# Optimization experiments

Measured on AMD Instinct MI355X. Metric: run time of the kernel, lower is better.

Reference implementation:

```python
import jax, jax.numpy as jnp
import numpy as np

B, INPUT, HIDDEN, MEM, SEQ, THETA, FFEAT = 8, 256, 256, 64, 2048, 2048.0, 64


def _expm(M):
    # scaling-and-squaring Taylor expm in float64 (replaces scipy cont2discrete internals)
    norm = np.linalg.norm(M, 1)
    s = max(0, int(np.ceil(np.log2(max(norm, 1e-16)))) + 1)
    A = M / (2.0 ** s)
    n = M.shape[0]
    E = np.eye(n)
    T = np.eye(n)
    for k in range(1, 30):
        T = T @ A / k
        E = E + T
    for _ in range(s):
        E = E @ E
    return E


def _lmu_fft_kernel(memory_size, theta, seq_len):
    # continuous-time LMU (A, B), discretized with ZOH (dt=1), as in cont2discrete
    Q = np.arange(memory_size, dtype=np.float64).reshape(-1, 1)
    R = (2 * Q + 1) / theta
    i, j = np.meshgrid(Q.ravel(), Q.ravel(), indexing='ij')
    A = R * np.where(i < j, -1.0, (-1.0) ** (i - j + 1))
    Bc = R * (-1.0) ** Q  # [m, 1]
    # ZOH via block matrix exponential: expm([[A,B],[0,0]]) = [[Ad,Bd],[0,I]]
    blk = np.zeros((memory_size + 1, memory_size + 1))
    blk[:memory_size, :memory_size] = A
    blk[:memory_size, memory_size:] = Bc
    M = _expm(blk)
    Ad = jnp.asarray(M[:memory_size, :memory_size], dtype=jnp.float32)
    Bd = jnp.asarray(M[:memory_size, memory_size:], dtype=jnp.float32)  # [m,1]
    # H[:, t] = Ad^t @ Bd
    def step(Ai, _):
        return Ad @ Ai, (Ai @ Bd)[:, 0]
    _, cols = jax.lax.scan(step, jnp.eye(memory_size, dtype=jnp.float32), None, length=seq_len)
    H = cols.T  # [m, S]
    return jnp.fft.rfft(H, n=2 * seq_len, axis=-1)  # [m, S+1] complex64


def setup_inputs() -> dict:
    key = jax.random.key(0)
    k1, k2, k3, k4, k5 = jax.random.split(key, 5)
    x = jax.random.normal(k1, (B, INPUT, SEQ), dtype=jnp.float32)
    Wu_w = jax.random.normal(k2, (FFEAT + HIDDEN, INPUT), dtype=jnp.float32) * (1.0 / np.sqrt(INPUT))
    Wu_b = jax.random.normal(k3, (FFEAT + HIDDEN,), dtype=jnp.float32) * 0.02
    Wh_w = jax.random.normal(k4, (HIDDEN, MEM * FFEAT), dtype=jnp.float32) * (1.0 / np.sqrt(MEM * FFEAT))
    Wh_b = jax.random.normal(k5, (HIDDEN,), dtype=jnp.float32) * 0.02
    fft_H = _lmu_fft_kernel(MEM, THETA, SEQ)
    return {"x": x, "Wu_w": Wu_w, "Wu_b": Wu_b, "Wh_w": Wh_w, "Wh_b": Wh_b, "fft_H": fft_H}


def reference(x, Wu_w, Wu_b, Wh_w, Wh_b, fft_H):
    batch, _, seq_len = x.shape
    hidden = Wh_w.shape[0]
    mem = fft_H.shape[0]
    # 1x1 conv == per-position GEMM
    out = jnp.einsum('oi,bis->bos', Wu_w, x) + Wu_b[None, :, None]  # [B, F+H, S]
    u = jax.nn.relu(out[:, hidden:])                                  # [B, F, S]
    fft_u = jnp.fft.rfft(u, n=2 * seq_len, axis=-1)                   # [B, F, S+1]
    temp = fft_u[:, :, None, :] * fft_H[None, None, :, :]             # [B, F, M, S+1]
    m = jnp.fft.irfft(temp, n=2 * seq_len, axis=-1)[..., :seq_len]    # [B, F, M, S]
    m = m.reshape(batch, -1, seq_len)                                 # [B, F*M, S]
    return jnp.einsum('oc,bcs->bos', Wh_w, m) + Wh_b[None, :, None] + out[:, :hidden]
```

## Files before the change

kernel.cpp:

```cpp
#include <hip/hip_runtime.h>
#include <hip/hip_bf16.h>
#include <math.h>

#define NB 8
#define NIN 256
#define NHID 256
#define NMEM 64
#define NSEQ 2048
#define NFEAT 64
#define NOUTCH 320
#define NFFT 4096
#define KBINS 2049

#define FFTU_SZ (NB * NFEAT * KBINS * 2)
#define FHD_SZ (NMEM * KBINS * 2)
#define TW_SZ (2048 * 2)
#define HBUF_SZ (NMEM * NSEQ)
#define FIXED_F (FFTU_SZ + FHD_SZ + TW_SZ + HBUF_SZ)
#define ZPERO_F (8 * KBINS * 2 * 2)

#define DMM   0
#define DTT0  4225
#define DTT1  8450
#define DEE0  12675
#define DEE1  16900
#define DPW   21125
#define DWV   (DPW + 6 * 4096)
#define DMK2  (DWV + 4096)

#define FIDX(i) ((i) + ((i) >> 5) + ((i) >> 10))
#define FFT_LDS 4240
#define HF_LDS 2120

__device__ __forceinline__ void fft4096_core(float* XR, float* XI,
                                             const float2* TWS, bool inverse) {
#pragma unroll 1
  for (int s = 1; s <= 12; ++s) {
    int half = 1 << (s - 1);
    int shift = 12 - s;
#pragma unroll
    for (int q = 0; q < 8; ++q) {
      int bf = threadIdx.x + q * 256;
      int j = bf & (half - 1);
      int base = ((bf >> (s - 1)) << s) + j;
      float2 w = TWS[j << shift];
      float wr = w.x, wi = inverse ? -w.y : w.y;
      int i0 = FIDX(base), i1 = FIDX(base + half);
      float ar = XR[i0], ai = XI[i0];
      float br = XR[i1], bi = XI[i1];
      float tr = wr * br - wi * bi, ti = wr * bi + wi * br;
      XR[i0] = ar + tr; XI[i0] = ai + ti;
      XR[i1] = ar - tr; XI[i1] = ai - ti;
    }
    __syncthreads();
  }
}

__device__ __forceinline__ void fft2048_core(float* XR, float* XI,
                                             const float2* TWS, bool inverse) {
#pragma unroll 1
  for (int s = 1; s <= 11; ++s) {
    int half = 1 << (s - 1);
    int shift = 12 - s;
#pragma unroll
    for (int q = 0; q < 4; ++q) {
      int bf = threadIdx.x + q * 256;
      int j = bf & (half - 1);
      int base = ((bf >> (s - 1)) << s) + j;
      float2 w = TWS[j << shift];
      float wr = w.x, wi = inverse ? -w.y : w.y;
      int i0 = FIDX(base), i1 = FIDX(base + half);
      float ar = XR[i0], ai = XI[i0];
      float br = XR[i1], bi = XI[i1];
      float tr = wr * br - wi * bi, ti = wr * bi + wi * br;
      XR[i0] = ar + tr; XI[i0] = ai + ti;
      XR[i1] = ar - tr; XI[i1] = ai - ti;
    }
    __syncthreads();
  }
}

__global__ void k0_tw(float2* __restrict__ tw) {
  int m = blockIdx.x * 256 + threadIdx.x;
  if (m < 2048) {
    double ang = -2.0 * 3.14159265358979323846 * (double)m / 4096.0;
    tw[m] = make_float2((float)cos(ang), (float)sin(ang));
  }
}

__global__ __launch_bounds__(256) void kinit(double* __restrict__ D) {
  int e = blockIdx.x * 256 + threadIdx.x;
  if (e < 4225) {
    int i = e / 65, j = e % 65;
    double val = 0.0;
    if (i < 64) {
      double R = (2.0 * i + 1.0) / 2048.0;
      if (j < 64) val = R * ((i < j) ? -1.0 : (((i - j) & 1) ? 1.0 : -1.0));
      else        val = R * ((i & 1) ? -1.0 : 1.0);
    }
    D[DMM + e] = 0.25 * val;
    double id = (i == j) ? 1.0 : 0.0;
    D[DTT0 + e] = id; D[DEE0 + e] = id;
  }
}
__global__ __launch_bounds__(256) void kmm65(const double* __restrict__ A,
                                             const double* __restrict__ B,
                                             double* __restrict__ C,
                                             double* __restrict__ E, double kd) {
  int e = blockIdx.x * 256 + threadIdx.x;
  if (e >= 4225) return;
  int i = e / 65, j = e % 65;
  const double* ar = A + i * 65;
  double dot = 0.0;
  for (int l = 0; l < 65; ++l) dot += ar[l] * B[l * 65 + j];
  dot /= kd;
  C[e] = dot;
  if (E) E[e] += dot;
}
__global__ __launch_bounds__(256) void kext(const double* __restrict__ E,
                                            double* __restrict__ D) {
  int e = blockIdx.x * 256 + threadIdx.x;
  if (e < 4096) {
    int i = e >> 6, j = e & 63;
    D[DPW + e] = (double)(float)E[i * 65 + j];
    D[DMK2 + e] = (i == j) ? 1.0 : 0.0;
  } else if (e < 4160) {
    int j = e - 4096;
    D[DWV + j] = (double)(float)E[j * 65 + 64];
  }
}
__global__ __launch_bounds__(256) void kmm64(const double* __restrict__ A,
                                             const double* __restrict__ B,
                                             double* __restrict__ C) {
  int e = blockIdx.x * 256 + threadIdx.x;
  int i = e >> 6, j = e & 63;
  double dot = 0.0;
  for (int l = 0; l < 64; ++l) dot += A[i * 64 + l] * B[l * 64 + j];
  C[e] = dot;
}
__global__ __launch_bounds__(256) void kwlev(const double* __restrict__ P,
                                             double* __restrict__ W, int b0) {
  int tot = 64 * b0;
  for (int e = threadIdx.x; e < tot; e += 256) {
    int t = e >> 6, i = e & 63;
    double dot = 0.0;
    for (int l = 0; l < 64; ++l) dot += P[i * 64 + l] * W[t * 64 + l];
    W[(size_t)(b0 + t) * 64 + i] = dot;
  }
}
__global__ __launch_bounds__(256) void kmk(const double* __restrict__ Q,
                                           const double* __restrict__ Src,
                                           double* __restrict__ Out) {
  int t = blockIdx.y;
  int e = blockIdx.x * 256 + threadIdx.x;
  int i = e >> 6, j = e & 63;
  const double* B = Src + (size_t)t * 4096;
  double dot = 0.0;
  for (int l = 0; l < 64; ++l) dot += Q[i * 64 + l] * B[l * 64 + j];
  Out[(size_t)t * 4096 + e] = dot;
}

__global__ __launch_bounds__(256) void kB_cols(const double* __restrict__ D,
                                               float* __restrict__ H) {
  const double* W = D + DWV;
  const double* Mrow = D + DMK2 + (size_t)blockIdx.x * 4096;
  __shared__ double Ms[4096];
  __shared__ double WssT[4096];
  const int tid = threadIdx.x;
  for (int e = tid; e < 4096; e += 256) {
    Ms[e] = Mrow[e];
    int r = e >> 6, j = e & 63;
    WssT[j * 64 + r] = W[e];
  }
  __syncthreads();
  const int c0 = blockIdx.x * 64;
  for (int e = tid; e < 4096; e += 256) {
    int i = e >> 6, r = e & 63;
    double dot = 0.0;
#pragma unroll 16
    for (int j = 0; j < 64; ++j) dot += Ms[i * 64 + j] * WssT[j * 64 + r];
    H[(size_t)i * NSEQ + c0 + r] = (float)dot;
  }
}

__global__ __launch_bounds__(256) void kC_fft(const float* __restrict__ H,
                                              const float2* __restrict__ tw,
                                              float* __restrict__ fHd) {
  __shared__ float XR[FFT_LDS], XI[FFT_LDS];
  __shared__ float2 TWS[2048];
  const int tid = threadIdx.x;
  const int mi = blockIdx.x;
  const float* src = H + (size_t)mi * NSEQ;
  for (int i = tid; i < NFFT; i += 256) { XR[FIDX(i)] = 0.f; XI[FIDX(i)] = 0.f; }
  for (int i = tid; i < 2048; i += 256) TWS[i] = tw[i];
  __syncthreads();
  for (int i = tid; i < NSEQ; i += 256) {
    int r = __brev((unsigned)i) >> 20;
    XR[FIDX(r)] = src[i];
  }
  __syncthreads();
  fft4096_core(XR, XI, TWS, false);
  float2* dst = (float2*)fHd + (size_t)mi * KBINS;
  for (int k = tid; k < KBINS; k += 256)
    dst[k] = make_float2(XR[FIDX(k)], XI[FIDX(k)]);
}

__global__ __launch_bounds__(256) void k1t(
    const float* __restrict__ x, const float* __restrict__ Wuw,
    const float* __restrict__ Wub, const float* __restrict__ Whb,
    float* __restrict__ dout, float* __restrict__ ubuf) {
  __shared__ float xs[32][128];
  __shared__ float wsh[32][68];
  const int tid = threadIdx.x;
  const int b = blockIdx.z;
  const int o0 = blockIdx.y * 64;
  const int s0 = blockIdx.x * 128;
  const int sx = tid & 15, oy = tid >> 4;
  float acc[4][8];
#pragma unroll
  for (int j = 0; j < 4; ++j)
#pragma unroll
    for (int l = 0; l < 8; ++l) acc[j][l] = 0.f;

  for (int i0 = 0; i0 < 256; i0 += 32) {
#pragma unroll
    for (int e4 = tid; e4 < 1024; e4 += 256) {
      int ii = e4 >> 5, ss4 = (e4 & 31) << 2;
      float4 v = *(const float4*)&x[(size_t)(b * NIN + i0 + ii) * NSEQ + s0 + ss4];
      *(float4*)&xs[ii][ss4] = v;
    }
#pragma unroll
    for (int e4 = tid; e4 < 512; e4 += 256) {
      int oj = e4 >> 3, ii4 = (e4 & 7) << 2;
      float4 v = *(const float4*)&Wuw[(o0 + oj) * NIN + i0 + ii4];
      wsh[ii4][oj] = v.x; wsh[ii4 + 1][oj] = v.y;
      wsh[ii4 + 2][oj] = v.z; wsh[ii4 + 3][oj] = v.w;
    }
    __syncthreads();
#pragma unroll 8
    for (int kk = 0; kk < 32; ++kk) {
      float4 a = *(const float4*)&wsh[kk][oy * 4];
      float4 b0 = *(const float4*)&xs[kk][sx * 4];
      float4 b1 = *(const float4*)&xs[kk][64 + sx * 4];
      float av[4] = {a.x, a.y, a.z, a.w};
      float bv[8] = {b0.x, b0.y, b0.z, b0.w, b1.x, b1.y, b1.z, b1.w};
#pragma unroll
      for (int j = 0; j < 4; ++j)
#pragma unroll
        for (int l = 0; l < 8; ++l) acc[j][l] = fmaf(av[j], bv[l], acc[j][l]);
    }
    __syncthreads();
  }
#pragma unroll
  for (int j = 0; j < 4; ++j) {
    int o = o0 + oy * 4 + j;
    if (o < NHID) {
      float bias = Wub[o] + Whb[o];
      size_t base = ((size_t)b * NHID + o) * NSEQ + s0;
      float4 v0 = make_float4(acc[j][0] + bias, acc[j][1] + bias,
                              acc[j][2] + bias, acc[j][3] + bias);
      float4 v1 = make_float4(acc[j][4] + bias, acc[j][5] + bias,
                              acc[j][6] + bias, acc[j][7] + bias);
      *(float4*)&dout[base + sx * 4] = v0;
      *(float4*)&dout[base + 64 + sx * 4] = v1;
    } else {
      float bias = Wub[o];
      size_t base = ((size_t)b * NFEAT + (o - NHID)) * NSEQ + s0;
      float4 v0 = make_float4(fmaxf(acc[j][0] + bias, 0.f), fmaxf(acc[j][1] + bias, 0.f),
                              fmaxf(acc[j][2] + bias, 0.f), fmaxf(acc[j][3] + bias, 0.f));
      float4 v1 = make_float4(fmaxf(acc[j][4] + bias, 0.f), fmaxf(acc[j][5] + bias, 0.f),
                              fmaxf(acc[j][6] + bias, 0.f), fmaxf(acc[j][7] + bias, 0.f));
      *(float4*)&ubuf[base + sx * 4] = v0;
      *(float4*)&ubuf[base + 64 + sx * 4] = v1;
    }
  }
}

__global__ __launch_bounds__(256) void k2h(
    const float* __restrict__ ubuf, const float2* __restrict__ tw,
    float* __restrict__ fftu) {
  __shared__ float XR[HF_LDS], XI[HF_LDS];
  __shared__ float2 TWS[2048];
  const int tid = threadIdx.x;
  const int b = blockIdx.x >> 6, f = blockIdx.x & 63;
  const float2* src2 = (const float2*)(ubuf + ((size_t)b * NFEAT + f) * NSEQ);
  for (int i = tid; i < 2048; i += 256) TWS[i] = tw[i];
  for (int n = tid; n < 2048; n += 256) {
    float2 y = (n < 1024) ? src2[n] : make_float2(0.f, 0.f);
    int r = __brev((unsigned)n) >> 21;
    XR[FIDX(r)] = y.x; XI[FIDX(r)] = y.y;
  }
  __syncthreads();
  fft2048_core(XR, XI, TWS, false);
  float2* dst = (float2*)fftu + ((size_t)b * NFEAT + f) * KBINS;
  for (int k = tid; k <= 2048; k += 256) {
    if (k < 2048) {
      int m = (2048 - k) & 2047;
      float yr = XR[FIDX(k)], yi = XI[FIDX(k)];
      float mr = XR[FIDX(m)], mi = XI[FIDX(m)];
      float ar = 0.5f * (yr + mr), ai = 0.5f * (yi - mi);
      float br = 0.5f * (yi + mi), bi = 0.5f * (mr - yr);
      float2 w = TWS[k];
      float Xr = ar + w.x * br - w.y * bi;
      float Xi = ai + w.x * bi + w.y * br;
      dst[k] = make_float2(Xr, Xi);
    } else {
      dst[2048] = make_float2(XR[FIDX(0)] - XI[FIDX(0)], 0.f);
    }
  }
}

#define WHT_STRIDE 132
#define K3_SMEM (64 * WHT_STRIDE + 64 * 65 * 2)
__global__ __launch_bounds__(256, 2) void k3p(
    const float* __restrict__ Whw, const float* __restrict__ fHd,
    const float* __restrict__ fftu, float* __restrict__ Zc,
    int ob0, int och, int nopair) {
  const int wgid = blockIdx.x;
  const int cxd = wgid & 7;
  const int sdx = wgid >> 3;
  const int opair = sdx % nopair;
  const int kt = cxd + 8 * (sdx / nopair);
  if (kt >= 33) return;

  __shared__ float smem[K3_SMEM];
  float* WhT = smem;
  float2 (*fHc)[65] = (float2(*)[65])(smem + 64 * WHT_STRIDE);
  float (*red)[64][33] = (float(*)[64][33])smem;
  const int tid = threadIdx.x;
  const int ol0 = opair * 2;
  const int o0 = ob0 + ol0;
  const int k0 = kt * 64;

  for (int e4 = tid; e4 < 2048; e4 += 256) {
    int ol = e4 >> 10;
    int idx4 = e4 & 1023;
    int f = idx4 >> 4, mi4 = idx4 & 15;
    float4 v = *(const float4*)&Whw[(size_t)(o0 + ol) * 4096 + f * 64 + mi4 * 4];
    WhT[(mi4 * 4 + 0) * WHT_STRIDE + f * 2 + ol] = v.x;
    WhT[(mi4 * 4 + 1) * WHT_STRIDE + f * 2 + ol] = v.y;
    WhT[(mi4 * 4 + 2) * WHT_STRIDE + f * 2 + ol] = v.z;
    WhT[(mi4 * 4 + 3) * WHT_STRIDE + f * 2 + ol] = v.w;
  }
  for (int e = tid; e < 4096; e += 256) {
    int mi = e >> 6, kk = e & 63;
    int k = k0 + kk;
    float2 v = make_float2(0.f, 0.f);
    if (k < KBINS) v = ((const float2*)fHd)[(size_t)mi * KBINS + k];
    fHc[mi][kk] = v;
  }
  __syncthreads();

  const int tk = tid & 63, g = tid >> 6;
  const int k = k0 + tk;
  const bool kok = (k < KBINS);
  const float2* fu2 = (const float2*)fftu;
  const size_t kb = (size_t)KBINS;

  float zr[2][8], zi[2][8];
#pragma unroll
  for (int ol = 0; ol < 2; ++ol)
#pragma unroll
    for (int b = 0; b < 8; ++b) { zr[ol][b] = 0.f; zi[ol][b] = 0.f; }

#pragma unroll 1
  for (int pass = 0; pass < 2; ++pass) {
    const int fbase = g * 16 + pass * 8;
    float2 ub[8], un[8];
#pragma unroll
    for (int b = 0; b < 8; ++b)
      ub[b] = kok ? fu2[((size_t)(b * NFEAT + fbase)) * kb + k]
                  : make_float2(0.f, 0.f);

    float G0r[8], G0i[8], G1r[8], G1i[8];
#pragma unroll
    for (int ff = 0; ff < 8; ++ff) { G0r[ff] = 0.f; G0i[ff] = 0.f;
                                     G1r[ff] = 0.f; G1i[ff] = 0.f; }

#pragma unroll 2
    for (int mi = 0; mi < 64; ++mi) {
      float2 h = fHc[mi][tk];
      const float* wrow = &WhT[mi * WHT_STRIDE + g * 32 + pass * 16];
#pragma unroll
      for (int ffp = 0; ffp < 4; ++ffp) {
        float4 w = *(const float4*)&wrow[ffp * 4];
        G0r[2 * ffp + 0] = fmaf(w.x, h.x, G0r[2 * ffp + 0]);
        G0i[2 * ffp + 0] = fmaf(w.x, h.y, G0i[2 * ffp + 0]);
        G1r[2 * ffp + 0] = fmaf(w.y, h.x, G1r[2 * ffp + 0]);
        G1i[2 * ffp + 0] = fmaf(w.y, h.y, G1i[2 * ffp + 0]);
        G0r[2 * ffp + 1] = fmaf(w.z, h.x, G0r[2 * ffp + 1]);
        G0i[2 * ffp + 1] = fmaf(w.z, h.y, G0i[2 * ffp + 1]);
        G1r[2 * ffp + 1] = fmaf(w.w, h.x, G1r[2 * ffp + 1]);
        G1i[2 * ffp + 1] = fmaf(w.w, h.y, G1i[2 * ffp + 1]);
      }
    }

#pragma unroll
    for (int ff = 0; ff < 8; ++ff) {
      if (ff < 7) {
#pragma unroll
        for (int b = 0; b < 8; ++b)
          un[b] = kok ? fu2[((size_t)(b * NFEAT + fbase + ff + 1)) * kb + k]
                      : make_float2(0.f, 0.f);
      }
      float gr0 = G0r[ff], gi0 = G0i[ff], gr1 = G1r[ff], gi1 = G1i[ff];
#pragma unroll
      for (int b = 0; b < 8; ++b) {
        float2 u = ub[b];
        zr[0][b] = fmaf(u.x, gr0, fmaf(-u.y, gi0, zr[0][b]));
        zi[0][b] = fmaf(u.x, gi0, fmaf( u.y, gr0, zi[0][b]));
        zr[1][b] = fmaf(u.x, gr1, fmaf(-u.y, gi1, zr[1][b]));
        zi[1][b] = fmaf(u.x, gi1, fmaf( u.y, gr1, zi[1][b]));
      }
#pragma unroll
      for (int b = 0; b < 8; ++b) ub[b] = un[b];
    }
  }
  __syncthreads();
#pragma unroll
  for (int ol = 0; ol < 2; ++ol)
#pragma unroll
    for (int b = 0; b < 8; ++b) {
      red[g][tk][(ol * 8 + b) * 2 + 0] = zr[ol][b];
      red[g][tk][(ol * 8 + b) * 2 + 1] = zi[ol][b];
    }
  __syncthreads();
  if (g == 0 && kok) {
    float2* Z2 = (float2*)Zc;
#pragma unroll
    for (int ol = 0; ol < 2; ++ol)
#pragma unroll
      for (int b = 0; b < 8; ++b) {
        int i0 = (ol * 8 + b) * 2;
        float sr = red[0][tk][i0]     + red[1][tk][i0]
                 + red[2][tk][i0]     + red[3][tk][i0];
        float si = red[0][tk][i0 + 1] + red[1][tk][i0 + 1]
                 + red[2][tk][i0 + 1] + red[3][tk][i0 + 1];
        Z2[((size_t)b * och + ol0 + ol) * KBINS + k] = make_float2(sr, si);
      }
  }
}

__global__ __launch_bounds__(256) void k4h(
    const float* __restrict__ Zc, const float2* __restrict__ tw,
    float* __restrict__ dout, int ob0, int och) {
  __shared__ float XR[HF_LDS], XI[HF_LDS];
  __shared__ float2 TWS[2048];
  const int tid = threadIdx.x;
  const int b = blockIdx.x / och, ol = blockIdx.x % och;
  const int o = ob0 + ol;
  const float2* Z2 = (const float2*)Zc + ((size_t)b * och + ol) * KBINS;
  for (int i = tid; i < 2048; i += 256) TWS[i] = tw[i];
  __syncthreads();
  for (int k = tid; k < 2048; k += 256) {
    float2 Xk = Z2[k];
    float2 Xm = Z2[2048 - k];
    float sr = Xk.x + Xm.x,  si = Xk.y - Xm.y;
    float dr = Xk.x - Xm.x,  di = Xk.y + Xm.y;
    float2 w = TWS[k];
    float tx = w.x, ty = -w.y;
    float cr = sr - (tx * di + ty * dr);
    float ci = si + (tx * dr - ty * di);
    int r = __brev((unsigned)k) >> 21;
    XR[FIDX(r)] = cr; XI[FIDX(r)] = ci;
  }
  __syncthreads();
  fft2048_core(XR, XI, TWS, true);
  const float inv = 1.0f / (float)NFFT;
  float2* drow = (float2*)(dout + ((size_t)b * NHID + o) * NSEQ);
  for (int n = tid; n < 1024; n += 256) {
    int idx = FIDX(n);
    float2 old = drow[n];
    drow[n] = make_float2(old.x + XR[idx] * inv, old.y + XI[idx] * inv);
  }
}

extern "C" void kernel_launch(void* const* d_in, const int* in_sizes, int n_in,
                              void* d_out, int out_size, void* d_ws, size_t ws_size,
                              hipStream_t stream) {
  const float* x   = (const float*)d_in[0];
  const float* Wuw = (const float*)d_in[1];
  const float* Wub = (const float*)d_in[2];
  const float* Whw = (const float*)d_in[3];
  const float* Whb = (const float*)d_in[4];
  float* out = (float*)d_out;
  float* ws  = (float*)d_ws;

  int och = 256;
  while (och > 32) {
    size_t need = ((size_t)FIXED_F + (size_t)och * 32784u) * 4u;
    if (need <= ws_size) break;
    och >>= 1;
  }
  const int noch = 256 / och;
  const int nopair = och / 2;
  const size_t z_f = (size_t)och * 32784u;

  float* fftu = ws;
  float* uz   = ws + FFTU_SZ;
  float* fHd  = uz + z_f;
  float2* tw  = (float2*)(fHd + FHD_SZ);
  float* Hbuf = (float*)tw + TW_SZ;
  double* D   = (double*)uz;

  k0_tw<<<8, 256, 0, stream>>>(tw);

  kinit<<<17, 256, 0, stream>>>(D);
  {
    double* t0 = D + DTT0;
    double* t1 = D + DTT1;
    for (int k = 1; k <= 8; ++k) {
      kmm65<<<17, 256, 0, stream>>>(t0, D + DMM, t1, D + DEE0, (double)k);
      double* tmp = t0; t0 = t1; t1 = tmp;
    }
  }
  kmm65<<<17, 256, 0, stream>>>(D + DEE0, D + DEE0, D + DEE1, (double*)nullptr, 1.0);
  kmm65<<<17, 256, 0, stream>>>(D + DEE1, D + DEE1, D + DEE0, (double*)nullptr, 1.0);
  kext<<<17, 256, 0, stream>>>(D + DEE0, D);
  for (int m = 1; m <= 5; ++m)
    kmm64<<<16, 256, 0, stream>>>(D + DPW + (m - 1) * 4096,
                                  D + DPW + (m - 1) * 4096,
                                  D + DPW + m * 4096);
  kmm64<<<16, 256, 0, stream>>>(D + DPW + 5 * 4096, D + DPW + 5 * 4096,
                                D + DMK2 + 4096);
  for (int m = 0; m <= 5; ++m)
    kwlev<<<1, 256, 0, stream>>>(D + DPW + m * 4096, D + DWV, 1 << m);
  for (int m = 1; m <= 4; ++m) {
    int b0 = 1 << m;
    kmm64<<<16, 256, 0, stream>>>(D + DMK2 + (size_t)(b0 / 2) * 4096,
                                  D + DMK2 + (size_t)(b0 / 2) * 4096,
                                  D + DMK2 + (size_t)b0 * 4096);
    int cnt = b0 - 1;
    kmk<<<dim3(16, cnt), 256, 0, stream>>>(D + DMK2 + (size_t)b0 * 4096,
                                           D + DMK2 + 4096,
                                           D + DMK2 + (size_t)(b0 + 1) * 4096);
  }

  kB_cols<<<32, 256, 0, stream>>>(D, Hbuf);
  kC_fft<<<NMEM, 256, 0, stream>>>(Hbuf, tw, fHd);
  k1t<<<dim3(NSEQ / 128, NOUTCH / 64, NB), 256, 0, stream>>>(x, Wuw, Wub, Whb, out, uz);
  k2h<<<NB * NFEAT, 256, 0, stream>>>(uz, tw, fftu);
  const int nwg3 = 8 * nopair * 5;
  for (int oc = 0; oc < noch; ++oc) {
    int ob0 = oc * och;
    k3p<<<nwg3, 256, 0, stream>>>(Whw, fHd, fftu, uz, ob0, och, nopair);
    k4h<<<NB * och, 256, 0, stream>>>(uz, tw, out, ob0, och);
  }
}
```

Before: 603.5 us.

## Fuse LMU matrix-exponential and power setup chain into one LDS-resident kernel

Replaces about 25 tiny launches (init, Taylor terms, squarings, power doublings, W-vector levels) with one single-workgroup kernel that keeps all 65x65 and 64x64 double matrices in shared memory. This removes per-launch overhead and global-memory round trips for the setup stage that builds the LMU impulse response. In exchange the whole chain runs on one CU with about 135KB of LDS, so the matmuls lose the parallelism of the multi-block launches. The 64x64 power matmuls now run serially inside one block.

Result: slower. 930.6 us (+54.2%).

```diff
diff --git a/kernel.cpp b/kernel.cpp
--- a/kernel.cpp
+++ b/kernel.cpp
@@ -17,16 +17,9 @@
 #define TW_SZ (2048 * 2)
 #define HBUF_SZ (NMEM * NSEQ)
 #define FIXED_F (FFTU_SZ + FHD_SZ + TW_SZ + HBUF_SZ)
-#define ZPERO_F (8 * KBINS * 2 * 2)
-
-#define DMM   0
-#define DTT0  4225
-#define DTT1  8450
-#define DEE0  12675
-#define DEE1  16900
-#define DPW   21125
-#define DWV   (DPW + 6 * 4096)
-#define DMK2  (DWV + 4096)
+
+#define DWV   0
+#define DMK2  4096
 
 #define FIDX(i) ((i) + ((i) >> 5) + ((i) >> 10))
 #define FFT_LDS 4240
@@ -88,9 +81,15 @@
   }
 }
 
-__global__ __launch_bounds__(256) void kinit(double* __restrict__ D) {
-  int e = blockIdx.x * 256 + threadIdx.x;
-  if (e < 4225) {
+__global__ __launch_bounds__(256, 1) void kAfuse(double* __restrict__ D) {
+  extern __shared__ double L[];
+  double* B0 = L;
+  double* B1 = L + 4225;
+  double* B2 = L + 8450;
+  double* B3 = L + 12675;
+  const int tid = threadIdx.x;
+
+  for (int e = tid; e < 4225; e += 256) {
     int i = e / 65, j = e % 65;
     double val = 0.0;
     if (i < 64) {
@@ -98,37 +97,77 @@
       if (j < 64) val = R * ((i < j) ? -1.0 : (((i - j) & 1) ? 1.0 : -1.0));
       else        val = R * ((i & 1) ? -1.0 : 1.0);
     }
-    D[DMM + e] = 0.25 * val;
+    B0[e] = 0.25 * val;
     double id = (i == j) ? 1.0 : 0.0;
-    D[DTT0 + e] = id; D[DEE0 + e] = id;
-  }
-}
-__global__ __launch_bounds__(256) void kmm65(const double* __restrict__ A,
-                                             const double* __restrict__ B,
-                                             double* __restrict__ C,
-                                             double* __restrict__ E, double kd) {
-  int e = blockIdx.x * 256 + threadIdx.x;
-  if (e >= 4225) return;
-  int i = e / 65, j = e % 65;
-  const double* ar = A + i * 65;
-  double dot = 0.0;
-  for (int l = 0; l < 65; ++l) dot += ar[l] * B[l * 65 + j];
-  dot /= kd;
-  C[e] = dot;
-  if (E) E[e] += dot;
-}
-__global__ __launch_bounds__(256) void kext(const double* __restrict__ E,
-                                            double* __restrict__ D) {
-  int e = blockIdx.x * 256 + threadIdx.x;
-  if (e < 4096) {
+    B1[e] = id; B2[e] = id;
+  }
+  __syncthreads();
+
+  {
+    double* T = B1; double* Tn = B3;
+    for (int k = 1; k <= 8; ++k) {
+      for (int e = tid; e < 4225; e += 256) {
+        int i = e / 65, j = e % 65;
+        double dot = 0.0;
+        for (int l = 0; l < 65; ++l) dot += T[i * 65 + l] * B0[l * 65 + j];
+        dot /= (double)k;
+        Tn[e] = dot;
+        B2[e] += dot;
+      }
+      __syncthreads();
+      double* tmp = T; T = Tn; Tn = tmp;
+    }
+  }
+  for (int e = tid; e < 4225; e += 256) {
+    int i = e / 65, j = e % 65;
+    double dot = 0.0;
+    for (int l = 0; l < 65; ++l) dot += B2[i * 65 + l] * B2[l * 65 + j];
+    B1[e] = dot;
+  }
+  __syncthreads();
+  for (int e = tid; e < 4225; e += 256) {
+    int i = e / 65, j = e % 65;
+    double dot = 0.0;
+    for (int l = 0; l < 65; ++l) dot += B1[i * 65 + l] * B1[l * 65 + j];
+    B3[e] = dot;
+  }
+  __syncthreads();
+  for (int e = tid; e < 4096; e += 256) {
     int i = e >> 6, j = e & 63;
-    D[DPW + e] = (double)(float)E[i * 65 + j];
-    D[DMK2 + e] = (i == j) ? 1.0 : 0.0;
-  } else if (e < 4160) {
-    int j = e - 4096;
-    D[DWV + j] = (double)(float)E[j * 65 + 64];
-  }
-}
+    B0[e] = (double)(float)B3[i * 65 + j];
+  }
+  if (tid < 64) B2[tid] = (double)(float)B3[tid * 65 + 64];
+  __syncthreads();
+  if (tid < 64) B3[tid] = B2[tid];
+  __syncthreads();
+  {
+    double* pwA = B0; double* pwB = B1;
+    for (int m = 0; m <= 5; ++m) {
+      int b0 = 1 << m;
+      for (int e = tid; e < 64 * b0; e += 256) {
+        int t = e >> 6, i = e & 63;
+        double dot = 0.0;
+        for (int l = 0; l < 64; ++l) dot += pwA[i * 64 + l] * B3[t * 64 + l];
+        B3[(size_t)(b0 + t) * 64 + i] = dot;
+      }
+      for (int e = tid; e < 4096; e += 256) {
+        int i = e >> 6, j = e & 63;
+        double dot = 0.0;
+        for (int l = 0; l < 64; ++l) dot += pwA[i * 64 + l] * pwA[l * 64 + j];
+        pwB[e] = dot;
+      }
+      __syncthreads();
+      double* tmp = pwA; pwA = pwB; pwB = tmp;
+    }
+    for (int e = tid; e < 4096; e += 256) {
+      D[DWV + e] = B3[e];
+      int i = e >> 6, j = e & 63;
+      D[DMK2 + e] = (i == j) ? 1.0 : 0.0;
+      D[DMK2 + 4096 + e] = pwA[e];
+    }
+  }
+}
+
 __global__ __launch_bounds__(256) void kmm64(const double* __restrict__ A,
                                              const double* __restrict__ B,
                                              double* __restrict__ C) {
@@ -137,16 +176,6 @@
   double dot = 0.0;
   for (int l = 0; l < 64; ++l) dot += A[i * 64 + l] * B[l * 64 + j];
   C[e] = dot;
-}
-__global__ __launch_bounds__(256) void kwlev(const double* __restrict__ P,
-                                             double* __restrict__ W, int b0) {
-  int tot = 64 * b0;
-  for (int e = threadIdx.x; e < tot; e += 256) {
-    int t = e >> 6, i = e & 63;
-    double dot = 0.0;
-    for (int l = 0; l < 64; ++l) dot += P[i * 64 + l] * W[t * 64 + l];
-    W[(size_t)(b0 + t) * 64 + i] = dot;
-  }
 }
 __global__ __launch_bounds__(256) void kmk(const double* __restrict__ Q,
                                            const double* __restrict__ Src,
@@ -505,26 +534,7 @@
 
   k0_tw<<<8, 256, 0, stream>>>(tw);
 
-  kinit<<<17, 256, 0, stream>>>(D);
-  {
-    double* t0 = D + DTT0;
-    double* t1 = D + DTT1;
-    for (int k = 1; k <= 8; ++k) {
-      kmm65<<<17, 256, 0, stream>>>(t0, D + DMM, t1, D + DEE0, (double)k);
-      double* tmp = t0; t0 = t1; t1 = tmp;
-    }
-  }
-  kmm65<<<17, 256, 0, stream>>>(D + DEE0, D + DEE0, D + DEE1, (double*)nullptr, 1.0);
-  kmm65<<<17, 256, 0, stream>>>(D + DEE1, D + DEE1, D + DEE0, (double*)nullptr, 1.0);
-  kext<<<17, 256, 0, stream>>>(D + DEE0, D);
-  for (int m = 1; m <= 5; ++m)
-    kmm64<<<16, 256, 0, stream>>>(D + DPW + (m - 1) * 4096,
-                                  D + DPW + (m - 1) * 4096,
-                                  D + DPW + m * 4096);
-  kmm64<<<16, 256, 0, stream>>>(D + DPW + 5 * 4096, D + DPW + 5 * 4096,
-                                D + DMK2 + 4096);
-  for (int m = 0; m <= 5; ++m)
-    kwlev<<<1, 256, 0, stream>>>(D + DPW + m * 4096, D + DWV, 1 << m);
+  kAfuse<<<1, 256, 4 * 4225 * sizeof(double), stream>>>(D);
   for (int m = 1; m <= 4; ++m) {
     int b0 = 1 << m;
     kmm64<<<16, 256, 0, stream>>>(D + DMK2 + (size_t)(b0 / 2) * 4096,
```
